# Performance work log

Measured on AMD Instinct MI355X. Metric: run time of the kernel, lower is better.

## Reference

```python
import jax, jax.numpy as jnp
import numpy as np
import math

B, L, D = 2, 2048, 1024
H = 16
DH = D // H


def setup_inputs() -> dict:
    key = jax.random.key(0)
    k1, k2, k3, k4 = jax.random.split(key, 4)
    s = 1.0 / math.sqrt(D)
    return {
        "x": jax.random.normal(k1, (B, L, D), dtype=jnp.float32),
        "w_in": jax.random.normal(k2, (3 * D, D), dtype=jnp.float32) * s,
        "b_in": jax.random.normal(k3, (3 * D,), dtype=jnp.float32) * 0.01,
        "w_out": jax.random.normal(k4, (D, D), dtype=jnp.float32) * s,
        "causal_mask": 1,
    }


def reference(x, w_in, b_in, w_out, causal_mask):
    b, seq_len, d = x.shape
    # fused QKV projection: (B,L,3D)
    qkv = x @ w_in.T + b_in
    q, k, v = jnp.split(qkv, 3, axis=-1)
    # (B,L,D) -> (B,H,L,DH)
    def heads(t):
        return t.reshape(b, seq_len, H, DH).transpose(0, 2, 1, 3)
    q, k, v = heads(q), heads(k), heads(v)
    scores = jnp.einsum("bhqd,bhkd->bhqk", q, k) / math.sqrt(DH)
    if causal_mask:
        causal = jnp.triu(jnp.ones((seq_len, seq_len), dtype=bool), k=1)
        scores = jnp.where(causal[None, None, :, :], jnp.float32(-1e9), scores)
    # stable softmax (amax-subtract as in original)
    weight = jax.nn.softmax(scores, axis=-1)
    out = jnp.einsum("bhqk,bhkd->bhqd", weight, v)
    out = out.transpose(0, 2, 1, 3).reshape(b, seq_len, d)
    return out @ w_out.T
```

## Files before the change

### kernel.cpp

```cpp
#include <hip/hip_runtime.h>
#include <hip/hip_bf16.h>

typedef __attribute__((ext_vector_type(8))) short short8;
typedef __attribute__((ext_vector_type(4))) short short4v;
typedef __attribute__((ext_vector_type(4))) float f32x4;

#define BB 2
#define LL 2048
#define DD 1024
#define HH 16
#define DHH 64
#define KK 1024
#define SCL 0.18033688011112042f
#define EXP2(x) __builtin_amdgcn_exp2f(x)

__device__ __forceinline__ void gload_lds16(const void* g, void* l) {
  __builtin_amdgcn_global_load_lds((const __attribute__((address_space(1))) void*)g,
                                   (__attribute__((address_space(3))) void*)l,
                                   16, 0, 0);
}

__device__ __forceinline__ unsigned short f2b(float x) {
  __hip_bfloat16 h = __float2bfloat16(x);
  return *reinterpret_cast<unsigned short*>(&h);
}

#define NX8  ((BB * LL * DD) / 8)
#define NWI8 ((3 * DD * DD) / 8)
#define NWO8 ((DD * DD) / 8)
__global__ void cvt_all(const float* __restrict__ x,
                        const float* __restrict__ w_in,
                        const float* __restrict__ w_out,
                        __hip_bfloat16* __restrict__ xb,
                        __hip_bfloat16* __restrict__ w_inb,
                        __hip_bfloat16* __restrict__ w_outb) {
  int i = blockIdx.x * blockDim.x + threadIdx.x;
  const float* src;
  __hip_bfloat16* dst;
  int j;
  if (i < NX8)              { src = x;     dst = xb;     j = i; }
  else if (i < NX8 + NWI8)  { src = w_in;  dst = w_inb;  j = i - NX8; }
  else                      { src = w_out; dst = w_outb; j = i - NX8 - NWI8; }
  const f32x4 a = ((const f32x4*)src)[j * 2];
  const f32x4 b = ((const f32x4*)src)[j * 2 + 1];
  short8 o;
#pragma unroll
  for (int k = 0; k < 4; ++k) o[k] = (short)f2b(a[k]);
#pragma unroll
  for (int k = 0; k < 4; ++k) o[4 + k] = (short)f2b(b[k]);
  ((short8*)dst)[j] = o;
}

template<bool QKV>
__global__ void gemm_bt(const __hip_bfloat16* __restrict__ A,
                        const __hip_bfloat16* __restrict__ Bm,
                        const float* __restrict__ bias,
                        __hip_bfloat16* __restrict__ Cq,
                        __hip_bfloat16* __restrict__ Ck,
                        __hip_bfloat16* __restrict__ Cv,
                        float* __restrict__ Cd,
                        int N, int nbn) {
  __shared__ __align__(16) char As[8192];
  __shared__ __align__(16) char Bs[8192];
  const int tid = threadIdx.x;
  const int lane = tid & 63, wid = tid >> 6;
  const int l15 = lane & 15, lhi = lane >> 4;
  const int wm = wid >> 1, wn = wid & 1;
  const int bn = blockIdx.x % nbn, bm = blockIdx.x / nbn;
  const int m0 = bm * 128, n0 = bn * 128;

  f32x4 acc[4][4] = {};

  for (int kt = 0; kt < KK / 32; ++kt) {
    const int k0 = kt * 32;
    __syncthreads();
#pragma unroll
    for (int j = 0; j < 2; ++j) {
      int c = wid * 128 + j * 64 + lane;
      int row = c >> 2;
      int ab = ((c & 3) * 16) ^ (((row >> 1) & 3) << 4);
      gload_lds16(A + (size_t)(m0 + row) * KK + k0 + (ab >> 1),
                  As + wid * 2048 + j * 1024);
    }
#pragma unroll
    for (int j = 0; j < 2; ++j) {
      int c = wid * 128 + j * 64 + lane;
      int row = c >> 2;
      int ab = ((c & 3) * 16) ^ (((row >> 1) & 3) << 4);
      gload_lds16(Bm + (size_t)(n0 + row) * KK + k0 + (ab >> 1),
                  Bs + wid * 2048 + j * 1024);
    }
    __syncthreads();

    short8 af[4], bf[4];
#pragma unroll
    for (int mf = 0; mf < 4; ++mf) {
      int row = wm * 64 + mf * 16 + l15;
      int byt = (lhi * 16) ^ (((row >> 1) & 3) << 4);
      af[mf] = *(const short8*)(As + row * 64 + byt);
    }
#pragma unroll
    for (int nf = 0; nf < 4; ++nf) {
      int row = wn * 64 + nf * 16 + l15;
      int byt = (lhi * 16) ^ (((row >> 1) & 3) << 4);
      bf[nf] = *(const short8*)(Bs + row * 64 + byt);
    }
#pragma unroll
    for (int mf = 0; mf < 4; ++mf)
#pragma unroll
      for (int nf = 0; nf < 4; ++nf)
        acc[mf][nf] = __builtin_amdgcn_mfma_f32_16x16x32_bf16(af[mf], bf[nf],
                                                              acc[mf][nf], 0, 0, 0);
  }

#pragma unroll
  for (int mf = 0; mf < 4; ++mf) {
#pragma unroll
    for (int nf = 0; nf < 4; ++nf) {
      const int n = n0 + wn * 64 + nf * 16 + l15;
      if constexpr (QKV) {
        const int sect = n >> 10;
        const int nn = n & 1023;
        const int h = nn >> 6, dh = nn & 63;
        const float bv = bias[n];
        const int m_base = m0 + wm * 64 + mf * 16 + lhi * 4;
        const int b = m_base >> 11, ml = m_base & 2047;
        if (sect == 2) {
          short4v v;
#pragma unroll
          for (int r = 0; r < 4; ++r) v[r] = (short)f2b(acc[mf][nf][r] + bv);
          *(short4v*)&Cv[(((size_t)(b * HH + h)) * DHH + dh) * LL + ml] = v;
        } else {
          __hip_bfloat16* dst = (sect == 0) ? Cq : Ck;
          const float scl = (sect == 0) ? SCL : 1.0f;
#pragma unroll
          for (int r = 0; r < 4; ++r)
            dst[(((size_t)(b * HH + h)) * LL + ml + r) * DHH + dh] =
                __float2bfloat16((acc[mf][nf][r] + bv) * scl);
        }
      } else {
#pragma unroll
        for (int r = 0; r < 4; ++r) {
          const int m = m0 + wm * 64 + mf * 16 + lhi * 4 + r;
          Cd[(size_t)m * N + n] = acc[mf][nf][r];
        }
      }
    }
  }
}

__global__ __launch_bounds__(128)
__attribute__((amdgpu_waves_per_eu(1, 4)))
void attn_fwd(
    const __hip_bfloat16* __restrict__ Q,
    const __hip_bfloat16* __restrict__ K,
    const __hip_bfloat16* __restrict__ VT,
    __hip_bfloat16* __restrict__ att,
    const int* __restrict__ maskp) {
  __shared__ __align__(16) char shm[8960];
  char* Pw = shm + (threadIdx.x >> 6) * 4096;
  float (*Ob)[68] = (float(*)[68])shm;
  float* Mb = (float*)(shm + 8704);
  float* Lb = (float*)(shm + 8832);
  const int tid = threadIdx.x;
  const int lane = tid & 63, wid = tid >> 6;
  const int l15 = lane & 15, lhi = lane >> 4;
  const int bid = blockIdx.x;
  const int strip = 63 - (bid >> 5);
  const int bh = bid & 31;
  const int causal = *maskp;
  const int r0 = strip * 32;
  const __hip_bfloat16* Qg = Q + (size_t)bh * LL * DHH;
  const __hip_bfloat16* Kg = K + (size_t)bh * LL * DHH;
  const __hip_bfloat16* VTg = VT + (size_t)bh * DHH * LL;
  const int swz = (l15 & 7) << 4;

  short8 aq[2][2];
#pragma unroll
  for (int mf = 0; mf < 2; ++mf)
#pragma unroll
    for (int ks = 0; ks < 2; ++ks)
      aq[mf][ks] = *(const short8*)(Qg + (size_t)(r0 + mf * 16 + l15) * DHH +
                                    ks * 32 + lhi * 8);

  f32x4 o[2][4] = {};
  float mrun[2] = {-1e30f, -1e30f};
  float lrun[2] = {0.0f, 0.0f};

  const int nt = causal ? ((r0 + 31) >> 6) + 1 : (LL / 64);
  const int hf = (nt + 1) >> 1;
  const int t0 = wid ? hf : 0;
  const int t1 = wid ? nt : hf;

  for (int t = t0; t < t1; ++t) {
    const int kv0 = t * 64;
    f32x4 s[2][4] = {};

    short8 kah[4];
#pragma unroll
    for (int nf = 0; nf < 4; ++nf)
      kah[nf] = *(const short8*)(Kg + (size_t)(kv0 + nf * 16 + l15) * DHH +
                                 lhi * 8);
    short8 bv[4][2];
#pragma unroll
    for (int nf = 0; nf < 4; ++nf)
#pragma unroll
      for (int ks = 0; ks < 2; ++ks)
        bv[nf][ks] = *(const short8*)(VTg + (size_t)(nf * 16 + l15) * LL +
                                      kv0 + ks * 32 + lhi * 8);

    __builtin_amdgcn_s_setprio(1);
#pragma unroll
    for (int nf = 0; nf < 4; ++nf) {
      s[0][nf] = __builtin_amdgcn_mfma_f32_16x16x32_bf16(kah[nf], aq[0][0], s[0][nf], 0, 0, 0);
      s[1][nf] = __builtin_amdgcn_mfma_f32_16x16x32_bf16(kah[nf], aq[1][0], s[1][nf], 0, 0, 0);
    }
    __builtin_amdgcn_s_setprio(0);
#pragma unroll
    for (int nf = 0; nf < 4; ++nf)
      kah[nf] = *(const short8*)(Kg + (size_t)(kv0 + nf * 16 + l15) * DHH +
                                 32 + lhi * 8);
    __builtin_amdgcn_s_setprio(1);
#pragma unroll
    for (int nf = 0; nf < 4; ++nf) {
      s[0][nf] = __builtin_amdgcn_mfma_f32_16x16x32_bf16(kah[nf], aq[0][1], s[0][nf], 0, 0, 0);
      s[1][nf] = __builtin_amdgcn_mfma_f32_16x16x32_bf16(kah[nf], aq[1][1], s[1][nf], 0, 0, 0);
    }
    __builtin_amdgcn_s_setprio(0);

    const bool needmask = causal && (kv0 + 63 > r0);
#pragma unroll
    for (int mf = 0; mf < 2; ++mf) {
      const int q = r0 + mf * 16 + l15;
      if (needmask)
#pragma unroll
        for (int nf = 0; nf < 4; ++nf) {
          const int kvb = kv0 + nf * 16 + lhi * 4;
#pragma unroll
          for (int r = 0; r < 4; ++r)
            if (kvb + r > q) s[mf][nf][r] = -1e30f;
        }
      f32x4 t4 = s[mf][0];
#pragma unroll
      for (int nf = 1; nf < 4; ++nf)
#pragma unroll
        for (int r = 0; r < 4; ++r) t4[r] = fmaxf(t4[r], s[mf][nf][r]);
      float pm = fmaxf(fmaxf(t4[0], t4[1]), fmaxf(t4[2], t4[3]));
      pm = fmaxf(pm, __shfl_xor(pm, 16, 64));
      pm = fmaxf(pm, __shfl_xor(pm, 32, 64));
      if (__any(pm > mrun[mf] + 8.0f)) {
        const float mnew = fmaxf(mrun[mf], pm);
        const float sc = EXP2(mrun[mf] - mnew);
        mrun[mf] = mnew;
        lrun[mf] *= sc;
#pragma unroll
        for (int nf = 0; nf < 4; ++nf)
#pragma unroll
          for (int r = 0; r < 4; ++r) o[mf][nf][r] *= sc;
      }
      float rs = 0.0f;
#pragma unroll
      for (int nf = 0; nf < 4; ++nf)
#pragma unroll
        for (int r = 0; r < 4; ++r) {
          float p = EXP2(s[mf][nf][r] - mrun[mf]);
          s[mf][nf][r] = p;
          rs += p;
        }
      rs += __shfl_xor(rs, 16, 64);
      rs += __shfl_xor(rs, 32, 64);
      lrun[mf] += rs;

      char* base = Pw + (mf * 16 + l15) * 128;
#pragma unroll
      for (int nf = 0; nf < 4; ++nf) {
        unsigned lo = (unsigned)f2b(s[mf][nf][0]) | ((unsigned)f2b(s[mf][nf][1]) << 16);
        unsigned hi = (unsigned)f2b(s[mf][nf][2]) | ((unsigned)f2b(s[mf][nf][3]) << 16);
        *(unsigned long long*)(base + ((nf * 32 + lhi * 8) ^ swz)) =
            (unsigned long long)lo | ((unsigned long long)hi << 32);
      }
    }

    __builtin_amdgcn_s_setprio(1);
#pragma unroll
    for (int mf = 0; mf < 2; ++mf) {
      const char* base = Pw + (mf * 16 + l15) * 128;
      short8 ap0 = *(const short8*)(base + ((lhi * 16) ^ swz));
      short8 ap1 = *(const short8*)(base + ((64 + lhi * 16) ^ swz));
#pragma unroll
      for (int nf = 0; nf < 4; ++nf) {
        o[mf][nf] = __builtin_amdgcn_mfma_f32_16x16x32_bf16(bv[nf][0], ap0, o[mf][nf], 0, 0, 0);
        o[mf][nf] = __builtin_amdgcn_mfma_f32_16x16x32_bf16(bv[nf][1], ap1, o[mf][nf], 0, 0, 0);
      }
    }
    __builtin_amdgcn_s_setprio(0);
  }

  __syncthreads();
  if (wid == 1) {
#pragma unroll
    for (int mf = 0; mf < 2; ++mf) {
      const int row = mf * 16 + l15;
      if (lhi == 0) { Mb[row] = mrun[mf]; Lb[row] = lrun[mf]; }
#pragma unroll
      for (int nf = 0; nf < 4; ++nf)
        *(f32x4*)&Ob[row][nf * 16 + lhi * 4] = o[mf][nf];
    }
  }
  __syncthreads();
  if (wid == 0) {
    const int b_ = bh >> 4, h = bh & 15;
#pragma unroll
    for (int mf = 0; mf < 2; ++mf) {
      const int row = mf * 16 + l15;
      const float m1 = Mb[row], l1 = Lb[row];
      const float mt = fmaxf(mrun[mf], m1);
      const float sc0 = EXP2(mrun[mf] - mt);
      const float sc1 = EXP2(m1 - mt);
      const float inv = 1.0f / (lrun[mf] * sc0 + l1 * sc1);
      __hip_bfloat16* dst = att + ((size_t)(b_ * LL + r0 + row)) * DD + h * DHH;
#pragma unroll
      for (int nf = 0; nf < 4; ++nf) {
        f32x4 ov = *(const f32x4*)&Ob[row][nf * 16 + lhi * 4];
        short4v pk;
#pragma unroll
        for (int r = 0; r < 4; ++r)
          pk[r] = (short)f2b((o[mf][nf][r] * sc0 + ov[r] * sc1) * inv);
        *(short4v*)(dst + nf * 16 + lhi * 4) = pk;
      }
    }
  }
}

extern "C" void kernel_launch(void* const* d_in, const int* in_sizes, int n_in,
                              void* d_out, int out_size, void* d_ws, size_t ws_size,
                              hipStream_t stream) {
  const float* x     = (const float*)d_in[0];
  const float* w_in  = (const float*)d_in[1];
  const float* b_in  = (const float*)d_in[2];
  const float* w_out = (const float*)d_in[3];
  const int* mask    = (const int*)d_in[4];
  float* out = (float*)d_out;

  char* ws = (char*)d_ws;
  const size_t MiB = 1024u * 1024u;
  __hip_bfloat16* xb    = (__hip_bfloat16*)(ws);
  __hip_bfloat16* w_inb = (__hip_bfloat16*)(ws + 8 * MiB);
  __hip_bfloat16* w_outb= (__hip_bfloat16*)(ws + 14 * MiB);
  __hip_bfloat16* Qb    = (__hip_bfloat16*)(ws + 16 * MiB);
  __hip_bfloat16* Kb    = (__hip_bfloat16*)(ws + 24 * MiB);
  __hip_bfloat16* Vtb   = (__hip_bfloat16*)(ws + 32 * MiB);
  __hip_bfloat16* att   = (__hip_bfloat16*)(ws + 40 * MiB);

  cvt_all<<<dim3(4096), dim3(256), 0, stream>>>(x, w_in, w_out, xb, w_inb, w_outb);

  gemm_bt<true><<<dim3(32 * 24), dim3(256), 0, stream>>>(
      xb, w_inb, b_in, Qb, Kb, Vtb, nullptr, 3072, 24);
  attn_fwd<<<dim3(2048), dim3(128), 0, stream>>>(Qb, Kb, Vtb, att, mask);
  gemm_bt<false><<<dim3(32 * 8), dim3(256), 0, stream>>>(
      att, w_outb, nullptr, nullptr, nullptr, nullptr, out, 1024, 8);
}
```

Baseline: 137.3 us.

## Pair causal strips per block, prefetch next K tile, restructure QK loop

Each attention block now handles two query strips (a late and an early one) so causal work per block is balanced, halving the grid to 1024 blocks. The K tile for the next iteration is prefetched into registers while the current one is processed, and the QK^T MFMAs are computed per row-fragment just before its softmax. The waves_per_eu hint is lowered to allow more registers for the prefetch buffers. This trades occupancy and grid size for load balance and latency hiding, and adds an extra barrier per strip.

```diff
diff --git a/kernel.cpp b/kernel.cpp
--- a/kernel.cpp
+++ b/kernel.cpp
@@ -150,7 +150,7 @@
 }
 
 __global__ __launch_bounds__(128)
-__attribute__((amdgpu_waves_per_eu(1, 4)))
+__attribute__((amdgpu_waves_per_eu(1, 3)))
 void attn_fwd(
     const __hip_bfloat16* __restrict__ Q,
     const __hip_bfloat16* __restrict__ K,
@@ -166,169 +166,179 @@
   const int lane = tid & 63, wid = tid >> 6;
   const int l15 = lane & 15, lhi = lane >> 4;
   const int bid = blockIdx.x;
-  const int strip = 63 - (bid >> 5);
+  const int pair = bid >> 5;
   const int bh = bid & 31;
   const int causal = *maskp;
-  const int r0 = strip * 32;
   const __hip_bfloat16* Qg = Q + (size_t)bh * LL * DHH;
   const __hip_bfloat16* Kg = K + (size_t)bh * LL * DHH;
   const __hip_bfloat16* VTg = VT + (size_t)bh * DHH * LL;
   const int swz = (l15 & 7) << 4;
-
-  short8 aq[2][2];
-#pragma unroll
-  for (int mf = 0; mf < 2; ++mf)
-#pragma unroll
-    for (int ks = 0; ks < 2; ++ks)
-      aq[mf][ks] = *(const short8*)(Qg + (size_t)(r0 + mf * 16 + l15) * DHH +
-                                    ks * 32 + lhi * 8);
-
-  f32x4 o[2][4] = {};
-  float mrun[2] = {-1e30f, -1e30f};
-  float lrun[2] = {0.0f, 0.0f};
-
-  const int nt = causal ? ((r0 + 31) >> 6) + 1 : (LL / 64);
-  const int hf = (nt + 1) >> 1;
-  const int t0 = wid ? hf : 0;
-  const int t1 = wid ? nt : hf;
-
-  for (int t = t0; t < t1; ++t) {
-    const int kv0 = t * 64;
-    f32x4 s[2][4] = {};
-
-    short8 kah[4];
+  const int b_ = bh >> 4, h = bh & 15;
+
+  for (int ph = 0; ph < 2; ++ph) {
+    const int strip = ph ? pair : (63 - pair);
+    const int r0 = strip * 32;
+
+    short8 aq[2][2];
+#pragma unroll
+    for (int mf = 0; mf < 2; ++mf)
+#pragma unroll
+      for (int ks = 0; ks < 2; ++ks)
+        aq[mf][ks] = *(const short8*)(Qg + (size_t)(r0 + mf * 16 + l15) * DHH +
+                                      ks * 32 + lhi * 8);
+
+    f32x4 o[2][4] = {};
+    float mrun[2] = {-1e30f, -1e30f};
+    float lrun[2] = {0.0f, 0.0f};
+
+    const int nt = causal ? ((r0 + 31) >> 6) + 1 : (LL / 64);
+    const int hf = (nt + 1) >> 1;
+    const int t0 = wid ? hf : 0;
+    const int t1 = wid ? nt : hf;
+
+    short8 ka[4][2];
 #pragma unroll
     for (int nf = 0; nf < 4; ++nf)
-      kah[nf] = *(const short8*)(Kg + (size_t)(kv0 + nf * 16 + l15) * DHH +
-                                 lhi * 8);
-    short8 bv[4][2];
-#pragma unroll
-    for (int nf = 0; nf < 4; ++nf)
 #pragma unroll
       for (int ks = 0; ks < 2; ++ks)
-        bv[nf][ks] = *(const short8*)(VTg + (size_t)(nf * 16 + l15) * LL +
-                                      kv0 + ks * 32 + lhi * 8);
-
-    __builtin_amdgcn_s_setprio(1);
-#pragma unroll
-    for (int nf = 0; nf < 4; ++nf) {
-      s[0][nf] = __builtin_amdgcn_mfma_f32_16x16x32_bf16(kah[nf], aq[0][0], s[0][nf], 0, 0, 0);
-      s[1][nf] = __builtin_amdgcn_mfma_f32_16x16x32_bf16(kah[nf], aq[1][0], s[1][nf], 0, 0, 0);
-    }
-    __builtin_amdgcn_s_setprio(0);
-#pragma unroll
-    for (int nf = 0; nf < 4; ++nf)
-      kah[nf] = *(const short8*)(Kg + (size_t)(kv0 + nf * 16 + l15) * DHH +
-                                 32 + lhi * 8);
-    __builtin_amdgcn_s_setprio(1);
-#pragma unroll
-    for (int nf = 0; nf < 4; ++nf) {
-      s[0][nf] = __builtin_amdgcn_mfma_f32_16x16x32_bf16(kah[nf], aq[0][1], s[0][nf], 0, 0, 0);
-      s[1][nf] = __builtin_amdgcn_mfma_f32_16x16x32_bf16(kah[nf], aq[1][1], s[1][nf], 0, 0, 0);
-    }
-    __builtin_amdgcn_s_setprio(0);
-
-    const bool needmask = causal && (kv0 + 63 > r0);
-#pragma unroll
-    for (int mf = 0; mf < 2; ++mf) {
-      const int q = r0 + mf * 16 + l15;
-      if (needmask)
+        ka[nf][ks] = *(const short8*)(Kg + (size_t)(t0 * 64 + nf * 16 + l15) * DHH +
+                                      ks * 32 + lhi * 8);
+
+    for (int t = t0; t < t1; ++t) {
+      const int kv0 = t * 64;
+      const int tn = (t + 1 < t1) ? t + 1 : t;
+      short8 kn[4][2];
+#pragma unroll
+      for (int nf = 0; nf < 4; ++nf)
+#pragma unroll
+        for (int ks = 0; ks < 2; ++ks)
+          kn[nf][ks] = *(const short8*)(Kg + (size_t)(tn * 64 + nf * 16 + l15) * DHH +
+                                        ks * 32 + lhi * 8);
+      short8 bv[4][2];
+#pragma unroll
+      for (int nf = 0; nf < 4; ++nf)
+#pragma unroll
+        for (int ks = 0; ks < 2; ++ks)
+          bv[nf][ks] = *(const short8*)(VTg + (size_t)(nf * 16 + l15) * LL +
+                                        kv0 + ks * 32 + lhi * 8);
+
+      const bool needmask = causal && (kv0 + 63 > r0);
+#pragma unroll
+      for (int mf = 0; mf < 2; ++mf) {
+        f32x4 s[4] = {};
+        __builtin_amdgcn_s_setprio(1);
+#pragma unroll
+        for (int ks = 0; ks < 2; ++ks)
+#pragma unroll
+          for (int nf = 0; nf < 4; ++nf)
+            s[nf] = __builtin_amdgcn_mfma_f32_16x16x32_bf16(ka[nf][ks], aq[mf][ks], s[nf], 0, 0, 0);
+        __builtin_amdgcn_s_setprio(0);
+
+        const int q = r0 + mf * 16 + l15;
+        if (needmask)
+#pragma unroll
+          for (int nf = 0; nf < 4; ++nf) {
+            const int kvb = kv0 + nf * 16 + lhi * 4;
+#pragma unroll
+            for (int r = 0; r < 4; ++r)
+              if (kvb + r > q) s[nf][r] = -1e30f;
+          }
+        f32x4 t4 = s[0];
+#pragma unroll
+        for (int nf = 1; nf < 4; ++nf)
+#pragma unroll
+          for (int r = 0; r < 4; ++r) t4[r] = fmaxf(t4[r], s[nf][r]);
+        float pm = fmaxf(fmaxf(t4[0], t4[1]), fmaxf(t4[2], t4[3]));
+        pm = fmaxf(pm, __shfl_xor(pm, 16, 64));
+        pm = fmaxf(pm, __shfl_xor(pm, 32, 64));
+        if (__any(pm > mrun[mf] + 8.0f)) {
+          const float mnew = fmaxf(mrun[mf], pm);
+          const float sc = EXP2(mrun[mf] - mnew);
+          mrun[mf] = mnew;
+          lrun[mf] *= sc;
+#pragma unroll
+          for (int nf = 0; nf < 4; ++nf)
+#pragma unroll
+            for (int r = 0; r < 4; ++r) o[mf][nf][r] *= sc;
+        }
+        float rs = 0.0f;
+#pragma unroll
+        for (int nf = 0; nf < 4; ++nf)
+#pragma unroll
+          for (int r = 0; r < 4; ++r) {
+            float p = EXP2(s[nf][r] - mrun[mf]);
+            s[nf][r] = p;
+            rs += p;
+          }
+        rs += __shfl_xor(rs, 16, 64);
+        rs += __shfl_xor(rs, 32, 64);
+        lrun[mf] += rs;
+
+        char* base = Pw + (mf * 16 + l15) * 128;
 #pragma unroll
         for (int nf = 0; nf < 4; ++nf) {
-          const int kvb = kv0 + nf * 16 + lhi * 4;
+          unsigned lo = (unsigned)f2b(s[nf][0]) | ((unsigned)f2b(s[nf][1]) << 16);
+          unsigned hi = (unsigned)f2b(s[nf][2]) | ((unsigned)f2b(s[nf][3]) << 16);
+          *(unsigned long long*)(base + ((nf * 32 + lhi * 8) ^ swz)) =
+              (unsigned long long)lo | ((unsigned long long)hi << 32);
+        }
+      }
+
+      __builtin_amdgcn_s_setprio(1);
+#pragma unroll
+      for (int mf = 0; mf < 2; ++mf) {
+        const char* base = Pw + (mf * 16 + l15) * 128;
+        short8 ap0 = *(const short8*)(base + ((lhi * 16) ^ swz));
+        short8 ap1 = *(const short8*)(base + ((64 + lhi * 16) ^ swz));
+#pragma unroll
+        for (int nf = 0; nf < 4; ++nf) {
+          o[mf][nf] = __builtin_amdgcn_mfma_f32_16x16x32_bf16(bv[nf][0], ap0, o[mf][nf], 0, 0, 0);
+          o[mf][nf] = __builtin_amdgcn_mfma_f32_16x16x32_bf16(bv[nf][1], ap1, o[mf][nf], 0, 0, 0);
+        }
+      }
+      __builtin_amdgcn_s_setprio(0);
+
+#pragma unroll
+      for (int nf = 0; nf < 4; ++nf)
+#pragma unroll
+        for (int ks = 0; ks < 2; ++ks)
+          ka[nf][ks] = kn[nf][ks];
+    }
+
+    __syncthreads();
+    if (wid == 1) {
+#pragma unroll
+      for (int mf = 0; mf < 2; ++mf) {
+        const int row = mf * 16 + l15;
+        if (lhi == 0) { Mb[row] = mrun[mf]; Lb[row] = lrun[mf]; }
+#pragma unroll
+        for (int nf = 0; nf < 4; ++nf)
+          *(f32x4*)&Ob[row][nf * 16 + lhi * 4] = o[mf][nf];
+      }
+    }
+    __syncthreads();
+    if (wid == 0) {
+#pragma unroll
+      for (int mf = 0; mf < 2; ++mf) {
+        const int row = mf * 16 + l15;
+        const float m1 = Mb[row], l1 = Lb[row];
+        const float mt = fmaxf(mrun[mf], m1);
+        const float sc0 = EXP2(mrun[mf] - mt);
+        const float sc1 = EXP2(m1 - mt);
+        const float inv = 1.0f / (lrun[mf] * sc0 + l1 * sc1);
+        __hip_bfloat16* dst = att + ((size_t)(b_ * LL + r0 + row)) * DD + h * DHH;
+#pragma unroll
+        for (int nf = 0; nf < 4; ++nf) {
+          f32x4 ov = *(const f32x4*)&Ob[row][nf * 16 + lhi * 4];
+          short4v pk;
 #pragma unroll
           for (int r = 0; r < 4; ++r)
-            if (kvb + r > q) s[mf][nf][r] = -1e30f;
-        }
-      f32x4 t4 = s[mf][0];
-#pragma unroll
-      for (int nf = 1; nf < 4; ++nf)
-#pragma unroll
-        for (int r = 0; r < 4; ++r) t4[r] = fmaxf(t4[r], s[mf][nf][r]);
-      float pm = fmaxf(fmaxf(t4[0], t4[1]), fmaxf(t4[2], t4[3]));
-      pm = fmaxf(pm, __shfl_xor(pm, 16, 64));
-      pm = fmaxf(pm, __shfl_xor(pm, 32, 64));
-      if (__any(pm > mrun[mf] + 8.0f)) {
-        const float mnew = fmaxf(mrun[mf], pm);
-        const float sc = EXP2(mrun[mf] - mnew);
-        mrun[mf] = mnew;
-        lrun[mf] *= sc;
-#pragma unroll
-        for (int nf = 0; nf < 4; ++nf)
-#pragma unroll
-          for (int r = 0; r < 4; ++r) o[mf][nf][r] *= sc;
-      }
-      float rs = 0.0f;
-#pragma unroll
-      for (int nf = 0; nf < 4; ++nf)
-#pragma unroll
-        for (int r = 0; r < 4; ++r) {
-          float p = EXP2(s[mf][nf][r] - mrun[mf]);
-          s[mf][nf][r] = p;
-          rs += p;
-        }
-      rs += __shfl_xor(rs, 16, 64);
-      rs += __shfl_xor(rs, 32, 64);
-      lrun[mf] += rs;
-
-      char* base = Pw + (mf * 16 + l15) * 128;
-#pragma unroll
-      for (int nf = 0; nf < 4; ++nf) {
-        unsigned lo = (unsigned)f2b(s[mf][nf][0]) | ((unsigned)f2b(s[mf][nf][1]) << 16);
-        unsigned hi = (unsigned)f2b(s[mf][nf][2]) | ((unsigned)f2b(s[mf][nf][3]) << 16);
-        *(unsigned long long*)(base + ((nf * 32 + lhi * 8) ^ swz)) =
-            (unsigned long long)lo | ((unsigned long long)hi << 32);
-      }
-    }
-
-    __builtin_amdgcn_s_setprio(1);
-#pragma unroll
-    for (int mf = 0; mf < 2; ++mf) {
-      const char* base = Pw + (mf * 16 + l15) * 128;
-      short8 ap0 = *(const short8*)(base + ((lhi * 16) ^ swz));
-      short8 ap1 = *(const short8*)(base + ((64 + lhi * 16) ^ swz));
-#pragma unroll
-      for (int nf = 0; nf < 4; ++nf) {
-        o[mf][nf] = __builtin_amdgcn_mfma_f32_16x16x32_bf16(bv[nf][0], ap0, o[mf][nf], 0, 0, 0);
-        o[mf][nf] = __builtin_amdgcn_mfma_f32_16x16x32_bf16(bv[nf][1], ap1, o[mf][nf], 0, 0, 0);
-      }
-    }
-    __builtin_amdgcn_s_setprio(0);
-  }
-
-  __syncthreads();
-  if (wid == 1) {
-#pragma unroll
-    for (int mf = 0; mf < 2; ++mf) {
-      const int row = mf * 16 + l15;
-      if (lhi == 0) { Mb[row] = mrun[mf]; Lb[row] = lrun[mf]; }
-#pragma unroll
-      for (int nf = 0; nf < 4; ++nf)
-        *(f32x4*)&Ob[row][nf * 16 + lhi * 4] = o[mf][nf];
-    }
-  }
-  __syncthreads();
-  if (wid == 0) {
-    const int b_ = bh >> 4, h = bh & 15;
-#pragma unroll
-    for (int mf = 0; mf < 2; ++mf) {
-      const int row = mf * 16 + l15;
-      const float m1 = Mb[row], l1 = Lb[row];
-      const float mt = fmaxf(mrun[mf], m1);
-      const float sc0 = EXP2(mrun[mf] - mt);
-      const float sc1 = EXP2(m1 - mt);
-      const float inv = 1.0f / (lrun[mf] * sc0 + l1 * sc1);
-      __hip_bfloat16* dst = att + ((size_t)(b_ * LL + r0 + row)) * DD + h * DHH;
-#pragma unroll
-      for (int nf = 0; nf < 4; ++nf) {
-        f32x4 ov = *(const f32x4*)&Ob[row][nf * 16 + lhi * 4];
-        short4v pk;
-#pragma unroll
-        for (int r = 0; r < 4; ++r)
-          pk[r] = (short)f2b((o[mf][nf][r] * sc0 + ov[r] * sc1) * inv);
-        *(short4v*)(dst + nf * 16 + lhi * 4) = pk;
-      }
-    }
+            pk[r] = (short)f2b((o[mf][nf][r] * sc0 + ov[r] * sc1) * inv);
+          *(short4v*)(dst + nf * 16 + lhi * 4) = pk;
+        }
+      }
+    }
+    __syncthreads();
   }
 }
 
@@ -356,7 +366,7 @@
 
   gemm_bt<true><<<dim3(32 * 24), dim3(256), 0, stream>>>(
       xb, w_inb, b_in, Qb, Kb, Vtb, nullptr, 3072, 24);
-  attn_fwd<<<dim3(2048), dim3(128), 0, stream>>>(Qb, Kb, Vtb, att, mask);
+  attn_fwd<<<dim3(1024), dim3(128), 0, stream>>>(Qb, Kb, Vtb, att, mask);
   gemm_bt<false><<<dim3(32 * 8), dim3(256), 0, stream>>>(
       att, w_outb, nullptr, nullptr, nullptr, nullptr, out, 1024, 8);
 }
```

Result: no change. 139.7 us (+1.7%).
